# Kernel optimization log

Measured on AMD Instinct MI355X. Metric: run time of the kernel, lower is better.

The kernel has to match this reference:

```python
import jax, jax.numpy as jnp
import numpy as np

NUM_EMBEDDINGS = 1024  # K
EMBEDDING_DIM = 64     # D
COMMITMENT_COST = 0.25


def setup_inputs() -> dict:
    key = jax.random.key(0)
    k1, k2 = jax.random.split(key)
    inputs = jax.random.normal(k1, (16, 4096, EMBEDDING_DIM), dtype=jnp.float32)
    # codebook init: uniform(-1/K, 1/K) as in nn.Embedding init in the module
    embedding = jax.random.uniform(
        k2, (NUM_EMBEDDINGS, EMBEDDING_DIM), dtype=jnp.float32,
        minval=-1.0 / NUM_EMBEDDINGS, maxval=1.0 / NUM_EMBEDDINGS)
    return {"inputs": inputs, "embedding": embedding}


def reference(inputs, embedding):
    input_shape = inputs.shape
    K = embedding.shape[0]
    flat = inputs.reshape(-1, embedding.shape[1])  # [N, D]

    distances = (jnp.sum(flat * flat, axis=1, keepdims=True)
                 + jnp.sum(embedding * embedding, axis=1)
                 - 2.0 * jnp.einsum('nd,kd->nk', flat, embedding))
    idx = jnp.argmin(distances, axis=1)                      # [N]
    encodings = jax.nn.one_hot(idx, K, dtype=flat.dtype)     # [N, K]
    quantized = embedding[idx]                               # [N, D] gather

    codebook_loss = jnp.mean((jax.lax.stop_gradient(quantized) - flat) ** 2)
    commitment_loss = jnp.mean((quantized - jax.lax.stop_gradient(flat)) ** 2)
    loss = codebook_loss + COMMITMENT_COST * commitment_loss

    # straight-through estimator
    quantized_st = flat + jax.lax.stop_gradient(quantized - flat)

    quantized_st = quantized_st.reshape(input_shape)
    encodings = encodings.reshape(*input_shape[:-1], K)
    return (quantized_st, encodings, loss, codebook_loss, commitment_loss)
```

## Files before the change

kernel.cpp:

```cpp
#include <hip/hip_runtime.h>
#include <float.h>

#define NVEC 65536
#define KCB  1024
#define DIM  64
#define ENC_OFF   ((size_t)NVEC * DIM)
#define LOSS_OFF  (ENC_OFF + (size_t)NVEC * KCB)
#define BAND 6e-5f

#define WS_SE_BOFF 64
#define WS_EH_BOFF 8192
#define WS_EL_BOFF (8192 + 131072)

typedef __attribute__((ext_vector_type(8))) short short8;
typedef __attribute__((ext_vector_type(4))) float f32x4;
typedef __attribute__((ext_vector_type(4))) unsigned int u32x4;

__device__ __forceinline__ unsigned short f2bf(float f) {
    unsigned u = __float_as_uint(f);
    return (unsigned short)((u + 0x7FFFu + ((u >> 16) & 1u)) >> 16);
}
__device__ __forceinline__ float bf2f(unsigned short h) {
    return __uint_as_float((unsigned)h << 16);
}

__global__ __launch_bounds__(256) void vq_prep(const float* __restrict__ emb,
                                               float* __restrict__ se,
                                               unsigned short* __restrict__ eh,
                                               unsigned short* __restrict__ el,
                                               float* __restrict__ loss3) {
    int g = blockIdx.x * 256 + threadIdx.x;
    if (g < 3) loss3[g] = 0.0f;
    if (g < KCB) {
        const f32x4* er = (const f32x4*)(emb + (size_t)g * DIM);
        double s0 = 0.0, s1 = 0.0, s2 = 0.0, s3 = 0.0;
#pragma unroll
        for (int i = 0; i < 16; i++) {
            f32x4 e = er[i];
            s0 = fma((double)e.x, (double)e.x, s0);
            s1 = fma((double)e.y, (double)e.y, s1);
            s2 = fma((double)e.z, (double)e.z, s2);
            s3 = fma((double)e.w, (double)e.w, s3);
        }
        se[g] = (float)((s0 + s1) + (s2 + s3));
    }
    for (int i = g; i < KCB * DIM; i += 64 * 256) {
        float v = emb[i];
        unsigned short h = f2bf(v);
        eh[i] = h;
        el[i] = f2bf(v - bf2f(h));
    }
}

__global__ __launch_bounds__(256) void vq_main(const float* __restrict__ x,
                                               const float* __restrict__ emb,
                                               const float* __restrict__ se,
                                               const unsigned short* __restrict__ eh,
                                               const unsigned short* __restrict__ el,
                                               float* __restrict__ outq,
                                               float* __restrict__ enc,
                                               float* __restrict__ lossacc) {
    __shared__ float sse[KCB];
    __shared__ int   sidx[64];
    __shared__ int   sflag[64];
    __shared__ int   scnt;
    __shared__ float red[4];
    __shared__ float sxrow[4][64];

    const int tid = threadIdx.x;
    const int wave = tid >> 6, lane = tid & 63;
    const int q = lane >> 4, c = lane & 15;

    if (tid == 0) scnt = 0;
    for (int t = tid; t < KCB; t += 256) sse[t] = se[t];

    const int vecm = blockIdx.x * 64 + wave * 16 + c;
    float xa[16];
    {
        const f32x4* xp = (const f32x4*)(x + (size_t)vecm * DIM);
        ((f32x4*)xa)[0] = xp[2 * q];
        ((f32x4*)xa)[1] = xp[2 * q + 1];
        ((f32x4*)xa)[2] = xp[8 + 2 * q];
        ((f32x4*)xa)[3] = xp[8 + 2 * q + 1];
    }
    short8 ah0, al0, ah1, al1;
#pragma unroll
    for (int j = 0; j < 8; j++) {
        unsigned short h0 = f2bf(xa[j]);
        ah0[j] = (short)h0;
        al0[j] = (short)f2bf(xa[j] - bf2f(h0));
        unsigned short h1 = f2bf(xa[8 + j]);
        ah1[j] = (short)h1;
        al1[j] = (short)f2bf(xa[8 + j] - bf2f(h1));
    }
    __syncthreads();

    float b1[4], b2[4];
    int i1[4];
#pragma unroll
    for (int r = 0; r < 4; r++) { b1[r] = FLT_MAX; b2[r] = FLT_MAX; i1[r] = 0; }

#pragma unroll 2
    for (int t = 0; t < 64; t++) {
        int kcur = t * 16 + c;
        const unsigned short* bph = eh + ((size_t)kcur << 6) + q * 8;
        const unsigned short* bpl = el + ((size_t)kcur << 6) + q * 8;
        short8 bh0 = *(const short8*)bph;
        short8 bh1 = *(const short8*)(bph + 32);
        short8 bl0 = *(const short8*)bpl;
        short8 bl1 = *(const short8*)(bpl + 32);
        f32x4 acc = {0.f, 0.f, 0.f, 0.f};
        acc = __builtin_amdgcn_mfma_f32_16x16x32_bf16(ah0, bh0, acc, 0, 0, 0);
        acc = __builtin_amdgcn_mfma_f32_16x16x32_bf16(ah1, bh1, acc, 0, 0, 0);
        acc = __builtin_amdgcn_mfma_f32_16x16x32_bf16(ah0, bl0, acc, 0, 0, 0);
        acc = __builtin_amdgcn_mfma_f32_16x16x32_bf16(ah1, bl1, acc, 0, 0, 0);
        acc = __builtin_amdgcn_mfma_f32_16x16x32_bf16(al0, bh0, acc, 0, 0, 0);
        acc = __builtin_amdgcn_mfma_f32_16x16x32_bf16(al1, bh1, acc, 0, 0, 0);
        float sek = sse[kcur];
#pragma unroll
        for (int r = 0; r < 4; r++) {
            float v = fmaf(-2.f, acc[r], sek);
            bool lt = v < b1[r];
            b2[r] = fminf(fmaxf(v, b1[r]), b2[r]);
            b1[r] = lt ? v : b1[r];
            i1[r] = lt ? kcur : i1[r];
        }
    }

#pragma unroll
    for (int m = 1; m <= 8; m <<= 1) {
#pragma unroll
        for (int r = 0; r < 4; r++) {
            float ob1 = __shfl_xor(b1[r], m, 64);
            float ob2 = __shfl_xor(b2[r], m, 64);
            int oi = __shfl_xor(i1[r], m, 64);
            float nb2 = fminf(fmaxf(b1[r], ob1), fminf(b2[r], ob2));
            if (ob1 < b1[r]) { b1[r] = ob1; i1[r] = oi; }
            b2[r] = nb2;
        }
    }
    if (c == 0) {
#pragma unroll
        for (int r = 0; r < 4; r++) {
            int row = wave * 16 + q * 4 + r;
            sidx[row] = i1[r];
            if (b2[r] - b1[r] < BAND) {
                int p = atomicAdd(&scnt, 1);
                sflag[p] = row;
            }
        }
    }
    __syncthreads();

    int cnt = scnt;
    for (int f = wave; f < cnt; f += 4) {
        int row = sflag[f];
        int n = blockIdx.x * 64 + row;
        if (lane < 16)
            ((f32x4*)sxrow[wave])[lane] = ((const f32x4*)(x + (size_t)n * DIM))[lane];
        const float* xr = sxrow[wave];

        float r8[8];
#pragma unroll
        for (int j = 0; j < 8; j++) r8[j] = 0.0f;
#pragma unroll
        for (int b = 0; b < 8; b++)
#pragma unroll
            for (int j = 0; j < 8; j++)
                r8[j] = __fadd_rn(r8[j], __fmul_rn(xr[8 * b + j], xr[8 * b + j]));
        float sx = __fadd_rn(
            __fadd_rn(__fadd_rn(r8[0], r8[1]), __fadd_rn(r8[2], r8[3])),
            __fadd_rn(__fadd_rn(r8[4], r8[5]), __fadd_rn(r8[6], r8[7])));

        float bd = FLT_MAX;
        int bk = lane * 16;
        for (int cc = 0; cc < 16; cc++) {
            int k = lane * 16 + cc;
            const f32x4* er = (const f32x4*)(emb + (size_t)k * DIM);
            double s0 = 0.0, s1 = 0.0, s2 = 0.0, s3 = 0.0;
#pragma unroll
            for (int i = 0; i < 16; i++) {
                f32x4 e = er[i];
                f32x4 xv = ((const f32x4*)xr)[i];
                s0 = fma((double)e.x, (double)xv.x, s0);
                s1 = fma((double)e.y, (double)xv.y, s1);
                s2 = fma((double)e.z, (double)xv.z, s2);
                s3 = fma((double)e.w, (double)xv.w, s3);
            }
            float dot32 = (float)((s0 + s1) + (s2 + s3));
            float t1 = __fadd_rn(sx, sse[k]);
            float d = __fsub_rn(t1, __fmul_rn(2.0f, dot32));
            if (d < bd) { bd = d; bk = k; }
        }
        for (int off = 32; off; off >>= 1) {
            float od = __shfl_down(bd, off);
            int ok = __shfl_down(bk, off);
            if (od < bd || (od == bd && ok < bk)) { bd = od; bk = ok; }
        }
        if (lane == 0) sidx[row] = bk;
    }
    __syncthreads();

    {
        int vec = tid >> 2, ch = tid & 3;
        int id = sidx[vec];
        const f32x4* ebp = (const f32x4*)(emb + (size_t)id * DIM) + ch * 4;
        const f32x4* xp = (const f32x4*)(x + (size_t)(blockIdx.x * 64 + vec) * DIM) + ch * 4;
        f32x4* op = (f32x4*)(outq + (size_t)(blockIdx.x * 64 + vec) * DIM) + ch * 4;
        float sq = 0.0f;
#pragma unroll
        for (int i = 0; i < 4; i++) {
            f32x4 e = ebp[i];
            f32x4 xv = xp[i];
            f32x4 d = e - xv;
            sq += d.x * d.x + d.y * d.y + d.z * d.z + d.w * d.w;
            __builtin_nontemporal_store(e, op + i);
        }
        for (int off = 32; off; off >>= 1) sq += __shfl_down(sq, off);
        if ((tid & 63) == 0) red[tid >> 6] = sq;
        __syncthreads();
        if (tid == 0) atomicAdd(lossacc, red[0] + red[1] + red[2] + red[3]);
    }

    f32x4* encb = (f32x4*)enc + (size_t)blockIdx.x * 64 * 256;
    for (int t = tid; t < 64 * 256; t += 256) {
        int id = sidx[t >> 8];
        int j = (t & 255) << 2;
        f32x4 v;
        v.x = (id == j + 0) ? 1.0f : 0.0f;
        v.y = (id == j + 1) ? 1.0f : 0.0f;
        v.z = (id == j + 2) ? 1.0f : 0.0f;
        v.w = (id == j + 3) ? 1.0f : 0.0f;
        __builtin_nontemporal_store(v, encb + t);
    }
}

__global__ void vq_fin(float* __restrict__ loss3) {
    if (threadIdx.x == 0 && blockIdx.x == 0) {
        float m = loss3[1] * (1.0f / (float)((size_t)NVEC * DIM));
        loss3[0] = 1.25f * m;
        loss3[1] = m;
        loss3[2] = m;
    }
}

extern "C" void kernel_launch(void* const* d_in, const int* in_sizes, int n_in,
                              void* d_out, int out_size, void* d_ws, size_t ws_size,
                              hipStream_t stream) {
    const float* x = (const float*)d_in[0];
    const float* emb = (const float*)d_in[1];
    float* out = (float*)d_out;
    float* se = (float*)((char*)d_ws + WS_SE_BOFF);
    unsigned short* eh = (unsigned short*)((char*)d_ws + WS_EH_BOFF);
    unsigned short* el = (unsigned short*)((char*)d_ws + WS_EL_BOFF);

    hipLaunchKernelGGL(vq_prep, dim3(64), dim3(256), 0, stream,
                       emb, se, eh, el, out + LOSS_OFF);
    hipLaunchKernelGGL(vq_main, dim3(NVEC / 64), dim3(256), 0, stream,
                       x, emb, se, eh, el, out, out + ENC_OFF, out + LOSS_OFF + 1);
    hipLaunchKernelGGL(vq_fin, dim3(1), dim3(64), 0, stream, out + LOSS_OFF);
}
```

Before: 484.4 us.

## Split VQ into screening and output-writing kernels with 32 rows per wave

The fused kernel becomes two. A screening kernel has each wave handle 32 rows instead of 16, so every codebook B-fragment load feeds two MFMA groups, and it writes the selected indices to workspace. A separate write kernel then emits the quantized output, the one-hot encodings and the loss. This halves codebook fragment traffic per row and separates the compute-bound search from the bandwidth-bound 256MB encoding write. The cost is an extra launch, a small index round-trip through global memory, fewer screening blocks (512), and more register pressure.

```diff
diff --git a/kernel.cpp b/kernel.cpp
--- a/kernel.cpp
+++ b/kernel.cpp
@@ -8,13 +8,13 @@
 #define LOSS_OFF  (ENC_OFF + (size_t)NVEC * KCB)
 #define BAND 6e-5f
 
-#define WS_SE_BOFF 64
-#define WS_EH_BOFF 8192
-#define WS_EL_BOFF (8192 + 131072)
+#define WS_SE_BOFF  64
+#define WS_EH_BOFF  8192
+#define WS_EL_BOFF  (8192 + 131072)
+#define WS_IDX_BOFF (WS_EL_BOFF + 131072)
 
 typedef __attribute__((ext_vector_type(8))) short short8;
 typedef __attribute__((ext_vector_type(4))) float f32x4;
-typedef __attribute__((ext_vector_type(4))) unsigned int u32x4;
 
 __device__ __forceinline__ unsigned short f2bf(float f) {
     unsigned u = __float_as_uint(f);
@@ -52,19 +52,16 @@
     }
 }
 
-__global__ __launch_bounds__(256) void vq_main(const float* __restrict__ x,
-                                               const float* __restrict__ emb,
-                                               const float* __restrict__ se,
-                                               const unsigned short* __restrict__ eh,
-                                               const unsigned short* __restrict__ el,
-                                               float* __restrict__ outq,
-                                               float* __restrict__ enc,
-                                               float* __restrict__ lossacc) {
+__global__ __launch_bounds__(256) void vq_screen(const float* __restrict__ x,
+                                                 const float* __restrict__ emb,
+                                                 const float* __restrict__ se,
+                                                 const unsigned short* __restrict__ eh,
+                                                 const unsigned short* __restrict__ el,
+                                                 unsigned short* __restrict__ idxg) {
     __shared__ float sse[KCB];
-    __shared__ int   sidx[64];
-    __shared__ int   sflag[64];
+    __shared__ int   sidx[128];
+    __shared__ int   sflag[128];
     __shared__ int   scnt;
-    __shared__ float red[4];
     __shared__ float sxrow[4][64];
 
     const int tid = threadIdx.x;
@@ -74,88 +71,100 @@
     if (tid == 0) scnt = 0;
     for (int t = tid; t < KCB; t += 256) sse[t] = se[t];
 
-    const int vecm = blockIdx.x * 64 + wave * 16 + c;
-    float xa[16];
-    {
-        const f32x4* xp = (const f32x4*)(x + (size_t)vecm * DIM);
+    const int rowbase = blockIdx.x * 128 + wave * 32;
+    short8 ah0[2], ah1[2], al0[2], al1[2];
+#pragma unroll
+    for (int s = 0; s < 2; s++) {
+        float xa[16];
+        const f32x4* xp = (const f32x4*)(x + (size_t)(rowbase + s * 16 + c) * DIM);
         ((f32x4*)xa)[0] = xp[2 * q];
         ((f32x4*)xa)[1] = xp[2 * q + 1];
         ((f32x4*)xa)[2] = xp[8 + 2 * q];
         ((f32x4*)xa)[3] = xp[8 + 2 * q + 1];
-    }
-    short8 ah0, al0, ah1, al1;
-#pragma unroll
-    for (int j = 0; j < 8; j++) {
-        unsigned short h0 = f2bf(xa[j]);
-        ah0[j] = (short)h0;
-        al0[j] = (short)f2bf(xa[j] - bf2f(h0));
-        unsigned short h1 = f2bf(xa[8 + j]);
-        ah1[j] = (short)h1;
-        al1[j] = (short)f2bf(xa[8 + j] - bf2f(h1));
-    }
-    __syncthreads();
-
-    float b1[4], b2[4];
-    int i1[4];
-#pragma unroll
-    for (int r = 0; r < 4; r++) { b1[r] = FLT_MAX; b2[r] = FLT_MAX; i1[r] = 0; }
-
+#pragma unroll
+        for (int j = 0; j < 8; j++) {
+            unsigned short h0 = f2bf(xa[j]);
+            ah0[s][j] = (short)h0;
+            al0[s][j] = (short)f2bf(xa[j] - bf2f(h0));
+            unsigned short h1 = f2bf(xa[8 + j]);
+            ah1[s][j] = (short)h1;
+            al1[s][j] = (short)f2bf(xa[8 + j] - bf2f(h1));
+        }
+    }
+    __syncthreads();
+
+    float b1[2][4], b2[2][4];
+    int i1[2][4];
+#pragma unroll
+    for (int s = 0; s < 2; s++)
+#pragma unroll
+        for (int r = 0; r < 4; r++) { b1[s][r] = FLT_MAX; b2[s][r] = FLT_MAX; i1[s][r] = 0; }
+
+    const unsigned short* ehq = eh + q * 8;
+    const unsigned short* elq = el + q * 8;
 #pragma unroll 2
     for (int t = 0; t < 64; t++) {
         int kcur = t * 16 + c;
-        const unsigned short* bph = eh + ((size_t)kcur << 6) + q * 8;
-        const unsigned short* bpl = el + ((size_t)kcur << 6) + q * 8;
+        const unsigned short* bph = ehq + ((size_t)kcur << 6);
+        const unsigned short* bpl = elq + ((size_t)kcur << 6);
         short8 bh0 = *(const short8*)bph;
         short8 bh1 = *(const short8*)(bph + 32);
         short8 bl0 = *(const short8*)bpl;
         short8 bl1 = *(const short8*)(bpl + 32);
-        f32x4 acc = {0.f, 0.f, 0.f, 0.f};
-        acc = __builtin_amdgcn_mfma_f32_16x16x32_bf16(ah0, bh0, acc, 0, 0, 0);
-        acc = __builtin_amdgcn_mfma_f32_16x16x32_bf16(ah1, bh1, acc, 0, 0, 0);
-        acc = __builtin_amdgcn_mfma_f32_16x16x32_bf16(ah0, bl0, acc, 0, 0, 0);
-        acc = __builtin_amdgcn_mfma_f32_16x16x32_bf16(ah1, bl1, acc, 0, 0, 0);
-        acc = __builtin_amdgcn_mfma_f32_16x16x32_bf16(al0, bh0, acc, 0, 0, 0);
-        acc = __builtin_amdgcn_mfma_f32_16x16x32_bf16(al1, bh1, acc, 0, 0, 0);
         float sek = sse[kcur];
 #pragma unroll
-        for (int r = 0; r < 4; r++) {
-            float v = fmaf(-2.f, acc[r], sek);
-            bool lt = v < b1[r];
-            b2[r] = fminf(fmaxf(v, b1[r]), b2[r]);
-            b1[r] = lt ? v : b1[r];
-            i1[r] = lt ? kcur : i1[r];
+        for (int s = 0; s < 2; s++) {
+            f32x4 acc = {0.f, 0.f, 0.f, 0.f};
+            acc = __builtin_amdgcn_mfma_f32_16x16x32_bf16(ah0[s], bh0, acc, 0, 0, 0);
+            acc = __builtin_amdgcn_mfma_f32_16x16x32_bf16(ah1[s], bh1, acc, 0, 0, 0);
+            acc = __builtin_amdgcn_mfma_f32_16x16x32_bf16(ah0[s], bl0, acc, 0, 0, 0);
+            acc = __builtin_amdgcn_mfma_f32_16x16x32_bf16(ah1[s], bl1, acc, 0, 0, 0);
+            acc = __builtin_amdgcn_mfma_f32_16x16x32_bf16(al0[s], bh0, acc, 0, 0, 0);
+            acc = __builtin_amdgcn_mfma_f32_16x16x32_bf16(al1[s], bh1, acc, 0, 0, 0);
+#pragma unroll
+            for (int r = 0; r < 4; r++) {
+                float v = fmaf(-2.f, acc[r], sek);
+                bool lt = v < b1[s][r];
+                b2[s][r] = fminf(fmaxf(v, b1[s][r]), b2[s][r]);
+                b1[s][r] = lt ? v : b1[s][r];
+                i1[s][r] = lt ? kcur : i1[s][r];
+            }
         }
     }
 
 #pragma unroll
     for (int m = 1; m <= 8; m <<= 1) {
 #pragma unroll
-        for (int r = 0; r < 4; r++) {
-            float ob1 = __shfl_xor(b1[r], m, 64);
-            float ob2 = __shfl_xor(b2[r], m, 64);
-            int oi = __shfl_xor(i1[r], m, 64);
-            float nb2 = fminf(fmaxf(b1[r], ob1), fminf(b2[r], ob2));
-            if (ob1 < b1[r]) { b1[r] = ob1; i1[r] = oi; }
-            b2[r] = nb2;
-        }
+        for (int s = 0; s < 2; s++)
+#pragma unroll
+            for (int r = 0; r < 4; r++) {
+                float ob1 = __shfl_xor(b1[s][r], m, 64);
+                float ob2 = __shfl_xor(b2[s][r], m, 64);
+                int oi = __shfl_xor(i1[s][r], m, 64);
+                float nb2 = fminf(fmaxf(b1[s][r], ob1), fminf(b2[s][r], ob2));
+                if (ob1 < b1[s][r]) { b1[s][r] = ob1; i1[s][r] = oi; }
+                b2[s][r] = nb2;
+            }
     }
     if (c == 0) {
 #pragma unroll
-        for (int r = 0; r < 4; r++) {
-            int row = wave * 16 + q * 4 + r;
-            sidx[row] = i1[r];
-            if (b2[r] - b1[r] < BAND) {
-                int p = atomicAdd(&scnt, 1);
-                sflag[p] = row;
-            }
-        }
+        for (int s = 0; s < 2; s++)
+#pragma unroll
+            for (int r = 0; r < 4; r++) {
+                int row = wave * 32 + s * 16 + q * 4 + r;
+                sidx[row] = i1[s][r];
+                if (b2[s][r] - b1[s][r] < BAND) {
+                    int p = atomicAdd(&scnt, 1);
+                    sflag[p] = row;
+                }
+            }
     }
     __syncthreads();
 
     int cnt = scnt;
     for (int f = wave; f < cnt; f += 4) {
         int row = sflag[f];
-        int n = blockIdx.x * 64 + row;
+        int n = blockIdx.x * 128 + row;
         if (lane < 16)
             ((f32x4*)sxrow[wave])[lane] = ((const f32x4*)(x + (size_t)n * DIM))[lane];
         const float* xr = sxrow[wave];
@@ -199,6 +208,22 @@
         }
         if (lane == 0) sidx[row] = bk;
     }
+    __syncthreads();
+
+    if (tid < 128)
+        idxg[blockIdx.x * 128 + tid] = (unsigned short)sidx[tid];
+}
+
+__global__ __launch_bounds__(256) void vq_write(const float* __restrict__ x,
+                                                const float* __restrict__ emb,
+                                                const unsigned short* __restrict__ idxg,
+                                                float* __restrict__ outq,
+                                                float* __restrict__ enc,
+                                                float* __restrict__ lossacc) {
+    __shared__ int sidx[64];
+    __shared__ float red[4];
+    const int tid = threadIdx.x;
+    if (tid < 64) sidx[tid] = idxg[blockIdx.x * 64 + tid];
     __syncthreads();
 
     {
@@ -253,10 +278,13 @@
     float* se = (float*)((char*)d_ws + WS_SE_BOFF);
     unsigned short* eh = (unsigned short*)((char*)d_ws + WS_EH_BOFF);
     unsigned short* el = (unsigned short*)((char*)d_ws + WS_EL_BOFF);
+    unsigned short* idxg = (unsigned short*)((char*)d_ws + WS_IDX_BOFF);
 
     hipLaunchKernelGGL(vq_prep, dim3(64), dim3(256), 0, stream,
                        emb, se, eh, el, out + LOSS_OFF);
-    hipLaunchKernelGGL(vq_main, dim3(NVEC / 64), dim3(256), 0, stream,
-                       x, emb, se, eh, el, out, out + ENC_OFF, out + LOSS_OFF + 1);
+    hipLaunchKernelGGL(vq_screen, dim3(NVEC / 128), dim3(256), 0, stream,
+                       x, emb, se, eh, el, idxg);
+    hipLaunchKernelGGL(vq_write, dim3(NVEC / 64), dim3(256), 0, stream,
+                       x, emb, idxg, out, out + ENC_OFF, out + LOSS_OFF + 1);
     hipLaunchKernelGGL(vq_fin, dim3(1), dim3(64), 0, stream, out + LOSS_OFF);
 }
```

After: 485.0 us. Within noise of the previous version (+0.1%).
